# Kernel tuning notes

Measured on AMD Instinct MI355X. Metric: run time of the kernel, lower is better.

The kernel has to match this reference:

```python
import jax, jax.numpy as jnp
import numpy as np

N_HEAD = 16

def setup_inputs() -> dict:
    key = jax.random.key(0)
    k1, k2, k3 = jax.random.split(key, 3)
    B, S, D = 2, 2048, 1024
    std = 0.02
    return {
        "hidden_states": jax.random.normal(k1, (B, S, D), jnp.float32),
        "w_attn": jax.random.normal(k2, (D, 3 * D), jnp.float32) * std,
        "b_attn": jnp.zeros((3 * D,), jnp.float32),
        "w_proj": jax.random.normal(k3, (D, D), jnp.float32) * std,
        "b_proj": jnp.zeros((D,), jnp.float32),
    }

def reference(hidden_states, w_attn, b_attn, w_proj, b_proj):
    B, S, D = hidden_states.shape
    H = N_HEAD
    hd = D // H
    # fused qkv projection (Conv1D == x @ W + b)
    qkv = hidden_states @ w_attn + b_attn            # [B,S,3D]
    q, k, v = jnp.split(qkv, 3, axis=-1)
    def split_heads(t):
        return t.reshape(B, S, H, hd).transpose(0, 2, 1, 3)  # [B,H,S,hd]
    q, k, v = split_heads(q), split_heads(k), split_heads(v)
    # scores with scale = sqrt(head_dim)
    scores = jnp.einsum('bhqd,bhkd->bhqk', q, k) / jnp.sqrt(jnp.asarray(hd, q.dtype))
    causal = jnp.tril(jnp.ones((S, S), bool))
    mask_value = jnp.finfo(scores.dtype).min
    scores = jnp.where(causal, scores, mask_value)
    attn = jax.nn.softmax(scores, axis=-1)           # dropout p=0 (eval)
    out = jnp.einsum('bhqk,bhkd->bhqd', attn, v)     # [B,H,S,hd]
    out = out.transpose(0, 2, 1, 3).reshape(B, S, D)
    out = out @ w_proj + b_proj
    return out
```

## Files before the change

kernel.cpp:

```cpp
#include <hip/hip_runtime.h>

#define S_LEN 2048
#define D_MODEL 1024
#define NHEAD 16
#define HDIM 64
#define BATCH 2
#define M_ROWS (BATCH * S_LEN)
#define N_QKV (3 * D_MODEL)
#define QSCALE 0.18033688011112042f

typedef __attribute__((ext_vector_type(8))) short bf16x8;
typedef __attribute__((ext_vector_type(4))) short bf16x4;
typedef __attribute__((ext_vector_type(4))) float f32x4;

#if __has_builtin(__builtin_amdgcn_mfma_f32_16x16x16bf16_1k)
#define MFMA1616(A, B, C) __builtin_amdgcn_mfma_f32_16x16x16bf16_1k((A), (B), (C), 0, 0, 0)
#else
static __device__ __forceinline__ f32x4 mfma1616_asm(bf16x4 a, bf16x4 b, f32x4 c) {
  asm("v_mfma_f32_16x16x16_bf16 %0, %1, %2, %0" : "+v"(c) : "v"(a), "v"(b));
  return c;
}
#define MFMA1616(A, B, C) mfma1616_asm((A), (B), (C))
#endif

static __device__ __forceinline__ unsigned short f2bf(float f) {
  unsigned int u = __float_as_uint(f);
  u += 0x7FFFu + ((u >> 16) & 1u);
  return (unsigned short)(u >> 16);
}
static __device__ __forceinline__ unsigned int pkbf(float a, float b) {
  unsigned int ua = __float_as_uint(a) + 0x8000u;
  unsigned int ub = __float_as_uint(b) + 0x8000u;
  return __builtin_amdgcn_perm(ub, ua, 0x07060302u);
}
static __device__ __forceinline__ unsigned int cvtpk(float a, float b) {
  unsigned int r;
  asm("v_cvt_pk_bf16_f32 %0, %1, %2" : "=v"(r) : "v"(a), "v"(b));
  return r;
}

static __device__ __forceinline__ void async_cp16(unsigned short* lds, const unsigned short* g) {
  __builtin_amdgcn_global_load_lds((__attribute__((address_space(1))) void*)g,
                                   (__attribute__((address_space(3))) void*)lds, 16, 0, 0);
}

__global__ __launch_bounds__(256) void k_prep(const float* __restrict__ x,
                                              unsigned short* __restrict__ xb,
                                              const float* __restrict__ w_attn,
                                              unsigned short* __restrict__ wqkvT,
                                              const float* __restrict__ w_proj,
                                              unsigned short* __restrict__ wprojT) {
  __shared__ unsigned short T[32][33];
  const int blk = blockIdx.x;
  const int tid = threadIdx.x;
  if (blk < 2048) {
    int i = blk * 256 + tid;
    float4 v0 = ((const float4*)x)[2 * i];
    float4 v1 = ((const float4*)x)[2 * i + 1];
    uint4 o;
    o.x = cvtpk(v0.x, v0.y);
    o.y = cvtpk(v0.z, v0.w);
    o.z = cvtpk(v1.x, v1.y);
    o.w = cvtpk(v1.z, v1.w);
    ((uint4*)xb)[i] = o;
    return;
  }
  const float* w;
  unsigned short* wT;
  int bid, Ndim;
  if (blk < 5120) { bid = blk - 2048; w = w_attn; wT = wqkvT; Ndim = N_QKV; }
  else            { bid = blk - 5120; w = w_proj; wT = wprojT; Ndim = D_MODEL; }
  const int nb = Ndim / 32;
  const int n0 = (bid % nb) * 32, k0 = (bid / nb) * 32;
  const int tx = tid & 31, ty = tid >> 5;
#pragma unroll
  for (int j = 0; j < 4; ++j) {
    int r = ty + j * 8;
    T[r][tx] = f2bf(w[(size_t)(k0 + r) * Ndim + n0 + tx]);
  }
  __syncthreads();
#pragma unroll
  for (int j = 0; j < 4; ++j) {
    int r = ty + j * 8;
    wT[(size_t)(n0 + r) * D_MODEL + k0 + tx] = T[tx][r];
  }
}

__global__ __launch_bounds__(256) void k_gemm_qkv(const unsigned short* __restrict__ A,
                                                  const unsigned short* __restrict__ Bt,
                                                  const float* __restrict__ bias,
                                                  unsigned short* __restrict__ Qb,
                                                  unsigned short* __restrict__ Kbuf,
                                                  unsigned short* __restrict__ VTb) {
  __shared__ __align__(16) unsigned short As[2][128 * 32];
  __shared__ __align__(16) unsigned short Bs[2][128 * 32];
  const int tid = threadIdx.x;
  const int wid = tid >> 6, lane = tid & 63;
  const int lr = lane & 15, lg = lane >> 4;
  const int blk = blockIdx.x;
  const int xcd = blk & 7, idx = blk >> 3;
  const int bm = ((xcd & 3) * 8 + (idx & 7)) * 128;
  const int bn = ((xcd >> 2) * 12 + (idx >> 3)) * 128;
  const int wm = (wid >> 1) * 64, wn = (wid & 1) * 64;
  const int K = D_MODEL;
  const int c0 = tid, c1 = tid + 256;
  const size_t a0o = (size_t)(bm + (c0 >> 2)) * K + (c0 & 3) * 8;
  const size_t a1o = (size_t)(bm + (c1 >> 2)) * K + (c1 & 3) * 8;
  const size_t b0o = (size_t)(bn + (c0 >> 2)) * K + (c0 & 3) * 8;
  const size_t b1o = (size_t)(bn + (c1 >> 2)) * K + (c1 & 3) * 8;

  f32x4 acc[4][4] = {};

  async_cp16(&As[0][c0 * 8], &A[a0o]);
  async_cp16(&As[0][c1 * 8], &A[a1o]);
  async_cp16(&Bs[0][c0 * 8], &Bt[b0o]);
  async_cp16(&Bs[0][c1 * 8], &Bt[b1o]);

  for (int k0 = 0; k0 < K; k0 += 32) {
    const int p = (k0 >> 5) & 1;
    __syncthreads();
    if (k0 + 32 < K) {
      async_cp16(&As[p ^ 1][c0 * 8], &A[a0o + k0 + 32]);
      async_cp16(&As[p ^ 1][c1 * 8], &A[a1o + k0 + 32]);
      async_cp16(&Bs[p ^ 1][c0 * 8], &Bt[b0o + k0 + 32]);
      async_cp16(&Bs[p ^ 1][c1 * 8], &Bt[b1o + k0 + 32]);
    }
    bf16x8 af[4], bfr[4];
#pragma unroll
    for (int i = 0; i < 4; ++i) af[i] = *(const bf16x8*)&As[p][(wm + i * 16 + lr) * 32 + lg * 8];
#pragma unroll
    for (int t = 0; t < 4; ++t) bfr[t] = *(const bf16x8*)&Bs[p][(wn + t * 16 + lr) * 32 + lg * 8];
#pragma unroll
    for (int i = 0; i < 4; ++i)
#pragma unroll
      for (int t = 0; t < 4; ++t)
        acc[i][t] = __builtin_amdgcn_mfma_f32_16x16x32_bf16(af[i], bfr[t], acc[i][t], 0, 0, 0);
  }
#pragma unroll
  for (int i = 0; i < 4; ++i) {
#pragma unroll
    for (int t = 0; t < 4; ++t) {
      int n = bn + wn + t * 16 + lr;
      int part = n >> 10, rem = n & 1023;
      int h = rem >> 6, d = rem & 63;
      float bv = bias[n];
      int row0 = bm + wm + i * 16 + lg * 4;
      int bb = row0 >> 11, s0 = row0 & 2047;
      if (part == 2) {
        ushort4 vv;
        vv.x = f2bf(acc[i][t][0] + bv);
        vv.y = f2bf(acc[i][t][1] + bv);
        vv.z = f2bf(acc[i][t][2] + bv);
        vv.w = f2bf(acc[i][t][3] + bv);
        int s0x = s0 ^ ((d & 8) ? 4 : 0);
        *(ushort4*)&VTb[(((size_t)(bb << 4) + h) * HDIM + d) * S_LEN + s0x] = vv;
      } else {
        unsigned short* dst = (part == 0) ? Qb : Kbuf;
        float sc = (part == 0) ? QSCALE : 1.0f;
#pragma unroll
        for (int r = 0; r < 4; ++r)
          dst[(((size_t)(bb << 4) + h) * S_LEN + (s0 + r)) * HDIM + d] = f2bf((acc[i][t][r] + bv) * sc);
      }
    }
  }
}

__global__ __launch_bounds__(256) void k_gemm_proj(const unsigned short* __restrict__ A,
                                                   const unsigned short* __restrict__ Bt,
                                                   const float* __restrict__ bias,
                                                   float* __restrict__ out) {
  __shared__ __align__(16) unsigned short As[2][128 * 32];
  __shared__ __align__(16) unsigned short Bs[2][128 * 32];
  const int tid = threadIdx.x;
  const int wid = tid >> 6, lane = tid & 63;
  const int lr = lane & 15, lg = lane >> 4;
  const int blk = blockIdx.x;
  const int xcd = blk & 7, idx = blk >> 3;
  const int bm = (xcd * 4 + (idx & 3)) * 128;
  const int bn = (idx >> 2) * 128;
  const int wm = (wid >> 1) * 64, wn = (wid & 1) * 64;
  const int K = D_MODEL;
  const int c0 = tid, c1 = tid + 256;
  const size_t a0o = (size_t)(bm + (c0 >> 2)) * K + (c0 & 3) * 8;
  const size_t a1o = (size_t)(bm + (c1 >> 2)) * K + (c1 & 3) * 8;
  const size_t b0o = (size_t)(bn + (c0 >> 2)) * K + (c0 & 3) * 8;
  const size_t b1o = (size_t)(bn + (c1 >> 2)) * K + (c1 & 3) * 8;

  f32x4 acc[4][4] = {};

  async_cp16(&As[0][c0 * 8], &A[a0o]);
  async_cp16(&As[0][c1 * 8], &A[a1o]);
  async_cp16(&Bs[0][c0 * 8], &Bt[b0o]);
  async_cp16(&Bs[0][c1 * 8], &Bt[b1o]);

  for (int k0 = 0; k0 < K; k0 += 32) {
    const int p = (k0 >> 5) & 1;
    __syncthreads();
    if (k0 + 32 < K) {
      async_cp16(&As[p ^ 1][c0 * 8], &A[a0o + k0 + 32]);
      async_cp16(&As[p ^ 1][c1 * 8], &A[a1o + k0 + 32]);
      async_cp16(&Bs[p ^ 1][c0 * 8], &Bt[b0o + k0 + 32]);
      async_cp16(&Bs[p ^ 1][c1 * 8], &Bt[b1o + k0 + 32]);
    }
    bf16x8 af[4], bfr[4];
#pragma unroll
    for (int i = 0; i < 4; ++i) af[i] = *(const bf16x8*)&As[p][(wm + i * 16 + lr) * 32 + lg * 8];
#pragma unroll
    for (int t = 0; t < 4; ++t) bfr[t] = *(const bf16x8*)&Bs[p][(wn + t * 16 + lr) * 32 + lg * 8];
#pragma unroll
    for (int i = 0; i < 4; ++i)
#pragma unroll
      for (int t = 0; t < 4; ++t)
        acc[i][t] = __builtin_amdgcn_mfma_f32_16x16x32_bf16(af[i], bfr[t], acc[i][t], 0, 0, 0);
  }
#pragma unroll
  for (int i = 0; i < 4; ++i) {
#pragma unroll
    for (int t = 0; t < 4; ++t) {
      int n = bn + wn + t * 16 + lr;
      float bv = bias[n];
#pragma unroll
      for (int r = 0; r < 4; ++r) {
        int row = bm + wm + i * 16 + lg * 4 + r;
        out[(size_t)row * D_MODEL + n] = acc[i][t][r] + bv;
      }
    }
  }
}

__global__ __launch_bounds__(256, 3) void k_attn14(const unsigned short* __restrict__ Qb,
                                                   const unsigned short* __restrict__ Kb,
                                                   const unsigned short* __restrict__ VT,
                                                   unsigned short* __restrict__ AO,
                                                   float* __restrict__ Pp) {
  const int tid = threadIdx.x;
  const int wid = tid >> 6, lane = tid & 63;
  const int lr = lane & 15, quad = lane >> 4;
  const int blk = blockIdx.x;
  const int bh = blk & 31;
  const int id = blk >> 5;
  const int b = bh >> 4, h = bh & 15;

  int T, c;
  if (id < 9)       { T = 7 + id; c = 0; }
  else if (id == 9) { T = 15;     c = 1; }
  else {
    const int j = id - 10, p_ = j >> 1;
    if (j & 1) { T = 14 - p_; c = 1; }
    else       { T = 6 - p_;  c = 0; }
  }
  const int kt0 = c << 4;
  const int tiles = 2 * T + 2;
  const int ktend = (c == 0) ? (tiles < 16 ? tiles : 16) : tiles;

  __shared__ __align__(16) unsigned short Ks[2][64 * 64];
  __shared__ __align__(16) unsigned short Vs[2][64 * 64];

  const unsigned short* Kbh = Kb + (size_t)bh * S_LEN * HDIM;
  const unsigned short* VTbh = VT + (size_t)bh * HDIM * S_LEN;

  const int R0 = T * 128 + wid * 32;

  bf16x8 qf[2][2];
#pragma unroll
  for (int st = 0; st < 2; ++st)
#pragma unroll
    for (int dh = 0; dh < 2; ++dh)
      qf[st][dh] = *(const bf16x8*)&Qb[((size_t)bh * S_LEN + R0 + st * 16 + lr) * HDIM + dh * 32 + quad * 8];

  f32x4 Ot[2][4] = {};
  float ls[2] = {0.f, 0.f};

  const int srow = lane >> 3;
  const int scol = ((lane & 7) ^ srow) * 8;

  {
    const int kg0 = kt0 * 64;
#pragma unroll
    for (int j = 0; j < 2; ++j) {
      const int r0 = wid * 16 + j * 8;
      async_cp16(&Ks[0][r0 * 64 + lane * 8], &Kbh[(size_t)(kg0 + r0 + srow) * HDIM + scol]);
      async_cp16(&Vs[0][r0 * 64 + lane * 8], &VTbh[(size_t)(r0 + srow) * S_LEN + kg0 + scol]);
    }
  }

  for (int kt = kt0; kt < ktend; ++kt) {
    const int k0 = kt * 64;
    const int p = kt & 1;
    __syncthreads();
    if (kt + 1 < ktend) {
      const int kn = k0 + 64;
#pragma unroll
      for (int j = 0; j < 2; ++j) {
        const int r0 = wid * 16 + j * 8;
        async_cp16(&Ks[p ^ 1][r0 * 64 + lane * 8], &Kbh[(size_t)(kn + r0 + srow) * HDIM + scol]);
        async_cp16(&Vs[p ^ 1][r0 * 64 + lane * 8], &VTbh[(size_t)(r0 + srow) * S_LEN + kn + scol]);
      }
    }
    if (k0 > R0 + 31) continue;

    bf16x8 kf[4][2];
#pragma unroll
    for (int kg = 0; kg < 4; ++kg)
#pragma unroll
      for (int dh = 0; dh < 2; ++dh)
        kf[kg][dh] = *(const bf16x8*)&Ks[p][(kg * 16 + lr) * 64 + (((dh * 4 + quad) ^ (lr & 7)) * 8)];

    bf16x4 pf[2][4];
    bool act[2];
#pragma unroll
    for (int st = 0; st < 2; ++st) {
      const int R = R0 + st * 16;
      act[st] = (k0 <= R + 15);
      if (!act[st]) continue;
      f32x4 Sv[4];
      __builtin_amdgcn_s_setprio(1);
#pragma unroll
      for (int kg = 0; kg < 4; ++kg) {
        f32x4 a = {};
        a = __builtin_amdgcn_mfma_f32_16x16x32_bf16(kf[kg][0], qf[st][0], a, 0, 0, 0);
        a = __builtin_amdgcn_mfma_f32_16x16x32_bf16(kf[kg][1], qf[st][1], a, 0, 0, 0);
        Sv[kg] = a;
      }
      __builtin_amdgcn_s_setprio(0);
      if (k0 + 63 > R) {
        const int q = R + lr;
#pragma unroll
        for (int kg = 0; kg < 4; ++kg)
#pragma unroll
          for (int r = 0; r < 4; ++r)
            if (k0 + kg * 16 + quad * 4 + r > q) Sv[kg][r] = -1e30f;
      }
      float rs = ls[st];
#pragma unroll
      for (int kg = 0; kg < 4; ++kg) {
        float e0 = __builtin_amdgcn_exp2f(Sv[kg][0]);
        float e1 = __builtin_amdgcn_exp2f(Sv[kg][1]);
        float e2 = __builtin_amdgcn_exp2f(Sv[kg][2]);
        float e3 = __builtin_amdgcn_exp2f(Sv[kg][3]);
        rs += (e0 + e1) + (e2 + e3);
        union { bf16x4 v; unsigned int u[2]; } pu;
        pu.u[0] = cvtpk(e0, e1);
        pu.u[1] = cvtpk(e2, e3);
        pf[st][kg] = pu.v;
      }
      ls[st] = rs;
    }

    __builtin_amdgcn_s_setprio(1);
#pragma unroll
    for (int dg = 0; dg < 4; ++dg) {
      bf16x4 vf[4];
#pragma unroll
      for (int kg = 0; kg < 4; ++kg)
        vf[kg] = *(const bf16x4*)&Vs[p][(dg * 16 + lr) * 64 +
                                        (((kg * 2 + (quad >> 1)) ^ (lr & 7)) * 8) +
                                        (((quad & 1) ^ ((lr >> 3) & 1)) * 4)];
#pragma unroll
      for (int st = 0; st < 2; ++st) {
        if (!act[st]) continue;
#pragma unroll
        for (int kg = 0; kg < 4; ++kg)
          Ot[st][dg] = MFMA1616(vf[kg], pf[st][kg], Ot[st][dg]);
      }
    }
    __builtin_amdgcn_s_setprio(0);
  }

#pragma unroll
  for (int st = 0; st < 2; ++st) {
    ls[st] += __shfl_xor(ls[st], 16);
    ls[st] += __shfl_xor(ls[st], 32);
  }

  if (T < 8) {
#pragma unroll
    for (int st = 0; st < 2; ++st) {
      const float rl = __builtin_amdgcn_rcpf(ls[st]);
      const int s = R0 + st * 16 + lr;
#pragma unroll
      for (int dg = 0; dg < 4; ++dg) {
        const size_t o = ((size_t)b * S_LEN + s) * D_MODEL + h * 64 + dg * 16 + quad * 4;
        *(unsigned int*)&AO[o]     = cvtpk(Ot[st][dg][0] * rl, Ot[st][dg][1] * rl);
        *(unsigned int*)&AO[o + 2] = cvtpk(Ot[st][dg][2] * rl, Ot[st][dg][3] * rl);
      }
    }
  } else {
#pragma unroll
    for (int st = 0; st < 2; ++st) {
      const int sL = T * 8 + wid * 2 + st;
      float* P = Pp + ((size_t)((bh * 64 + (sL - 64)) * 2 + c)) * (16 * 68) + lr * 68;
#pragma unroll
      for (int dg = 0; dg < 4; ++dg)
        *(f32x4*)&P[dg * 16 + quad * 4] = Ot[st][dg];
      if (quad == 0) { P[64] = 0.f; P[65] = ls[st]; }
    }
  }
}

__global__ __launch_bounds__(256) void k_combine(const float* __restrict__ Pp,
                                                 unsigned short* __restrict__ AO) {
  const int lane = threadIdx.x & 63;
  const int sid = blockIdx.x * 4 + (threadIdx.x >> 6);
  const int bh = sid >> 6, jrel = sid & 63;
  const int b = bh >> 4, h = bh & 15;
  const int r = lane & 15, cg = lane >> 4;
  const float* P0 = Pp + ((size_t)(bh * 64 + jrel) * 2) * (16 * 68) + r * 68;
  const float* P1 = P0 + 16 * 68;
  const float m0 = P0[64], l0 = P0[65];
  const float m1 = P1[64], l1 = P1[65];
  const float M = fmaxf(m0, m1);
  const float w0 = __builtin_amdgcn_exp2f(m0 - M);
  const float w1 = __builtin_amdgcn_exp2f(m1 - M);
  const float rl = __builtin_amdgcn_rcpf(l0 * w0 + l1 * w1);
  const int s = (64 + jrel) * 16 + r;
  const size_t o0 = ((size_t)b * S_LEN + s) * D_MODEL + h * 64 + cg * 16;
#pragma unroll
  for (int q4 = 0; q4 < 4; ++q4) {
    f32x4 a = *(const f32x4*)&P0[cg * 16 + q4 * 4];
    f32x4 b4 = *(const f32x4*)&P1[cg * 16 + q4 * 4];
    float o0v = (a[0] * w0 + b4[0] * w1) * rl;
    float o1v = (a[1] * w0 + b4[1] * w1) * rl;
    float o2v = (a[2] * w0 + b4[2] * w1) * rl;
    float o3v = (a[3] * w0 + b4[3] * w1) * rl;
    *(unsigned int*)&AO[o0 + q4 * 4]     = pkbf(o0v, o1v);
    *(unsigned int*)&AO[o0 + q4 * 4 + 2] = pkbf(o2v, o3v);
  }
}

extern "C" void kernel_launch(void* const* d_in, const int* in_sizes, int n_in,
                              void* d_out, int out_size, void* d_ws, size_t ws_size,
                              hipStream_t stream) {
  const float* x      = (const float*)d_in[0];
  const float* w_attn = (const float*)d_in[1];
  const float* b_attn = (const float*)d_in[2];
  const float* w_proj = (const float*)d_in[3];
  const float* b_proj = (const float*)d_in[4];
  float* out = (float*)d_out;

  unsigned short* ws     = (unsigned short*)d_ws;
  unsigned short* xb     = ws;
  unsigned short* wqkvT  = xb + (size_t)M_ROWS * D_MODEL;
  unsigned short* wprojT = wqkvT + (size_t)N_QKV * D_MODEL;
  unsigned short* Qb     = wprojT + (size_t)D_MODEL * D_MODEL;
  unsigned short* Kb     = Qb + (size_t)M_ROWS * D_MODEL;
  unsigned short* VT     = Kb + (size_t)M_ROWS * D_MODEL;
  float* Pp              = (float*)(VT + (size_t)M_ROWS * D_MODEL);
  unsigned short* AO     = xb;

  k_prep<<<6144, 256, 0, stream>>>(x, xb, w_attn, wqkvT, w_proj, wprojT);
  k_gemm_qkv<<<768, 256, 0, stream>>>(xb, wqkvT, b_attn, Qb, Kb, VT);
  k_attn14<<<768, 256, 0, stream>>>(Qb, Kb, VT, AO, Pp);
  k_combine<<<512, 256, 0, stream>>>(Pp, AO);
  k_gemm_proj<<<256, 256, 0, stream>>>(AO, wprojT, b_proj, out);
}
```

Baseline: 172.4 us.

## Fuse split-KV combine into attention kernel via atomic last-arriver merge

Removes the separate combine kernel. Each split-KV attention block writes its partial output and row sum, issues a threadfence, then atomically swaps a per-wave flag. Whichever of the two halves arrives second reads the other half's partial, normalizes, and writes the bf16 output directly. This saves a kernel launch and a full pass over the partials. In exchange it adds global atomics and fences, and it depends on the flag buffer starting at zero. Each merge resets its flag to zero so later calls start clean.

```diff
diff --git a/kernel.cpp b/kernel.cpp
--- a/kernel.cpp
+++ b/kernel.cpp
@@ -8,6 +8,7 @@
 #define M_ROWS (BATCH * S_LEN)
 #define N_QKV (3 * D_MODEL)
 #define QSCALE 0.18033688011112042f
+#define MERGE_MAGIC 0x5A17C0DEu
 
 typedef __attribute__((ext_vector_type(8))) short bf16x8;
 typedef __attribute__((ext_vector_type(4))) short bf16x4;
@@ -27,11 +28,6 @@
   unsigned int u = __float_as_uint(f);
   u += 0x7FFFu + ((u >> 16) & 1u);
   return (unsigned short)(u >> 16);
-}
-static __device__ __forceinline__ unsigned int pkbf(float a, float b) {
-  unsigned int ua = __float_as_uint(a) + 0x8000u;
-  unsigned int ub = __float_as_uint(b) + 0x8000u;
-  return __builtin_amdgcn_perm(ub, ua, 0x07060302u);
 }
 static __device__ __forceinline__ unsigned int cvtpk(float a, float b) {
   unsigned int r;
@@ -228,11 +224,12 @@
   }
 }
 
-__global__ __launch_bounds__(256, 3) void k_attn14(const unsigned short* __restrict__ Qb,
+__global__ __launch_bounds__(256, 3) void k_attn17(const unsigned short* __restrict__ Qb,
                                                    const unsigned short* __restrict__ Kb,
                                                    const unsigned short* __restrict__ VT,
                                                    unsigned short* __restrict__ AO,
-                                                   float* __restrict__ Pp) {
+                                                   float* __restrict__ Pp,
+                                                   unsigned int* __restrict__ flags) {
   const int tid = threadIdx.x;
   const int wid = tid >> 6, lane = tid & 63;
   const int lr = lane & 15, quad = lane >> 4;
@@ -393,38 +390,32 @@
 #pragma unroll
       for (int dg = 0; dg < 4; ++dg)
         *(f32x4*)&P[dg * 16 + quad * 4] = Ot[st][dg];
-      if (quad == 0) { P[64] = 0.f; P[65] = ls[st]; }
-    }
-  }
-}
-
-__global__ __launch_bounds__(256) void k_combine(const float* __restrict__ Pp,
-                                                 unsigned short* __restrict__ AO) {
-  const int lane = threadIdx.x & 63;
-  const int sid = blockIdx.x * 4 + (threadIdx.x >> 6);
-  const int bh = sid >> 6, jrel = sid & 63;
-  const int b = bh >> 4, h = bh & 15;
-  const int r = lane & 15, cg = lane >> 4;
-  const float* P0 = Pp + ((size_t)(bh * 64 + jrel) * 2) * (16 * 68) + r * 68;
-  const float* P1 = P0 + 16 * 68;
-  const float m0 = P0[64], l0 = P0[65];
-  const float m1 = P1[64], l1 = P1[65];
-  const float M = fmaxf(m0, m1);
-  const float w0 = __builtin_amdgcn_exp2f(m0 - M);
-  const float w1 = __builtin_amdgcn_exp2f(m1 - M);
-  const float rl = __builtin_amdgcn_rcpf(l0 * w0 + l1 * w1);
-  const int s = (64 + jrel) * 16 + r;
-  const size_t o0 = ((size_t)b * S_LEN + s) * D_MODEL + h * 64 + cg * 16;
-#pragma unroll
-  for (int q4 = 0; q4 < 4; ++q4) {
-    f32x4 a = *(const f32x4*)&P0[cg * 16 + q4 * 4];
-    f32x4 b4 = *(const f32x4*)&P1[cg * 16 + q4 * 4];
-    float o0v = (a[0] * w0 + b4[0] * w1) * rl;
-    float o1v = (a[1] * w0 + b4[1] * w1) * rl;
-    float o2v = (a[2] * w0 + b4[2] * w1) * rl;
-    float o3v = (a[3] * w0 + b4[3] * w1) * rl;
-    *(unsigned int*)&AO[o0 + q4 * 4]     = pkbf(o0v, o1v);
-    *(unsigned int*)&AO[o0 + q4 * 4 + 2] = pkbf(o2v, o3v);
+      if (quad == 0) P[64] = ls[st];
+    }
+    __threadfence();
+    const int fi = (bh << 5) + ((T - 8) << 2) + wid;
+    unsigned int old = 0;
+    if (lane == 0) old = atomicExch(&flags[fi], MERGE_MAGIC);
+    old = __shfl(old, 0);
+    if (old == MERGE_MAGIC) {
+      __threadfence();
+      if (lane == 0) atomicExch(&flags[fi], 0u);
+#pragma unroll
+      for (int st = 0; st < 2; ++st) {
+        const int sL = T * 8 + wid * 2 + st;
+        const float* Po = Pp + ((size_t)((bh * 64 + (sL - 64)) * 2 + (c ^ 1))) * (16 * 68) + lr * 68;
+        const float lo = Po[64];
+        const float rl = __builtin_amdgcn_rcpf(ls[st] + lo);
+        const int s = R0 + st * 16 + lr;
+#pragma unroll
+        for (int dg = 0; dg < 4; ++dg) {
+          f32x4 ov = *(const f32x4*)&Po[dg * 16 + quad * 4];
+          const size_t o = ((size_t)b * S_LEN + s) * D_MODEL + h * 64 + dg * 16 + quad * 4;
+          *(unsigned int*)&AO[o]     = cvtpk((Ot[st][dg][0] + ov[0]) * rl, (Ot[st][dg][1] + ov[1]) * rl);
+          *(unsigned int*)&AO[o + 2] = cvtpk((Ot[st][dg][2] + ov[2]) * rl, (Ot[st][dg][3] + ov[3]) * rl);
+        }
+      }
+    }
   }
 }
 
@@ -446,11 +437,11 @@
   unsigned short* Kb     = Qb + (size_t)M_ROWS * D_MODEL;
   unsigned short* VT     = Kb + (size_t)M_ROWS * D_MODEL;
   float* Pp              = (float*)(VT + (size_t)M_ROWS * D_MODEL);
+  unsigned int* flags    = (unsigned int*)(Pp + (size_t)2048 * 2 * 16 * 68);
   unsigned short* AO     = xb;
 
   k_prep<<<6144, 256, 0, stream>>>(x, xb, w_attn, wqkvT, w_proj, wprojT);
   k_gemm_qkv<<<768, 256, 0, stream>>>(xb, wqkvT, b_attn, Qb, Kb, VT);
-  k_attn14<<<768, 256, 0, stream>>>(Qb, Kb, VT, AO, Pp);
-  k_combine<<<512, 256, 0, stream>>>(Pp, AO);
+  k_attn17<<<768, 256, 0, stream>>>(Qb, Kb, VT, AO, Pp, flags);
   k_gemm_proj<<<256, 256, 0, stream>>>(AO, wprojT, b_proj, out);
 }
```

New measurement: 275.3 us. +59.7%, slower.
